# Kernel tuning notes

Measured on AMD Instinct MI355X. Metric: run time of the kernel, lower is better.

Reference implementation:

```python
import jax, jax.numpy as jnp
import numpy as np

N_HEAD = 4
D_MODEL = 256
FEAT_DIM = 256
D_K = D_MODEL // N_HEAD  # 64
TEMP = float(np.sqrt(D_K))
LN_EPS = 1e-5


def setup_inputs() -> dict:
    key = jax.random.key(0)
    ks = jax.random.split(key, 12)
    B, N_src, N_ngh = 2048, 1, 128
    src = jax.random.normal(ks[0], (B, N_src, FEAT_DIM), dtype=jnp.float32)
    seq = jax.random.normal(ks[1], (B, N_ngh, FEAT_DIM), dtype=jnp.float32)
    mask = jax.random.randint(ks[2], (B, N_ngh), 0, 2) > 0
    s_qk = np.sqrt(2.0 / (D_MODEL + D_K))
    w_qs = jax.random.normal(ks[3], (N_HEAD * D_K, D_MODEL), dtype=jnp.float32) * s_qk
    w_ks = jax.random.normal(ks[4], (N_HEAD * D_K, D_MODEL), dtype=jnp.float32) * s_qk
    w_vs = jax.random.normal(ks[5], (N_HEAD * D_K, D_MODEL), dtype=jnp.float32) * s_qk
    fc_w = jax.random.normal(ks[6], (D_MODEL, N_HEAD * D_K), dtype=jnp.float32) * 0.05
    fc_b = jnp.zeros((D_MODEL,), dtype=jnp.float32)
    ln_g = jnp.ones((D_MODEL,), dtype=jnp.float32)
    ln_b = jnp.zeros((D_MODEL,), dtype=jnp.float32)
    fc1_w = jax.random.normal(ks[7], (FEAT_DIM, 2 * D_MODEL), dtype=jnp.float32) * 0.05
    fc1_b = jnp.zeros((FEAT_DIM,), dtype=jnp.float32)
    fc2_w = jax.random.normal(ks[8], (FEAT_DIM, FEAT_DIM), dtype=jnp.float32) * 0.05
    fc2_b = jnp.zeros((FEAT_DIM,), dtype=jnp.float32)
    return {"src": src, "seq": seq, "mask": mask, "w_qs": w_qs, "w_ks": w_ks,
            "w_vs": w_vs, "fc_w": fc_w, "fc_b": fc_b, "ln_g": ln_g, "ln_b": ln_b,
            "fc1_w": fc1_w, "fc1_b": fc1_b, "fc2_w": fc2_w, "fc2_b": fc2_b}


def _forward(src, seq, mask, w_qs, w_ks, w_vs, fc_w, fc_b, ln_g, ln_b,
             fc1_w, fc1_b, fc2_w, fc2_b):
    B, N_src, _ = src.shape
    N_ngh = seq.shape[1]
    nn_ = N_ngh // N_src
    # projections (dropout is identity in eval mode)
    qh = (src @ w_qs.T).reshape(B, N_src, N_HEAD, D_K)              # bshd
    kh = (seq @ w_ks.T).reshape(B, N_src, nn_, N_HEAD, D_K)        # bsnhd
    vh = (seq @ w_vs.T).reshape(B, N_src, nn_, N_HEAD, D_K)
    scores = jnp.einsum('bshd,bsnhd->bshn', qh, kh) / TEMP          # [B,Ns,H,nn]
    # Replicate original mask layout exactly: attn rows are flat in (b,s,h)
    # order, but mask was built with .repeat(n_head,1,1) -> head-major tiling.
    flat = scores.reshape(B * N_src * N_HEAD, nn_)
    mask_rep = jnp.tile(mask.reshape(B * N_src, nn_), (N_HEAD, 1))  # [H*B*Ns, nn]
    flat = jnp.where(mask_rep, -1e10, flat)
    attn = jax.nn.softmax(flat, axis=-1).reshape(B, N_src, N_HEAD, nn_)
    out = jnp.einsum('bshn,bsnhd->bshd', attn, vh).reshape(B, N_src, N_HEAD * D_K)
    out = out @ fc_w.T + fc_b
    x = out + src  # residual (q == src since pos_dim == 0)
    mu = jnp.mean(x, axis=-1, keepdims=True)
    var = jnp.mean(jnp.square(x - mu), axis=-1, keepdims=True)
    x = (x - mu) * jax.lax.rsqrt(var + LN_EPS) * ln_g + ln_b
    # MergeLayer (non_linear=True)
    h = jax.nn.relu(jnp.concatenate([x, src], axis=-1) @ fc1_w.T + fc1_b)
    z = h @ fc2_w.T + fc2_b                                        # [B,Ns,feat]
    return z, attn


def reference(src, seq, mask, w_qs, w_ks, w_vs, fc_w, fc_b, ln_g, ln_b,
              fc1_w, fc1_b, fc2_w, fc2_b):
    return _forward(src, seq, mask, w_qs, w_ks, w_vs, fc_w, fc_b, ln_g, ln_b,
                    fc1_w, fc1_b, fc2_w, fc2_b)
```

## Files before the change

kernel.cpp:

```cpp
#include <hip/hip_runtime.h>

typedef unsigned int uint32;
typedef unsigned short ushort16;

#define DI __device__ __forceinline__

#define BATCH 2048
#define NN    128
#define DM    256
#define NH    4
#define DK    64

#define GLOAD_LDS16(g, s) \
  __builtin_amdgcn_global_load_lds( \
      (const __attribute__((address_space(1))) unsigned int*)(g), \
      (__attribute__((address_space(3))) unsigned int*)(s), 16, 0, 0)

DI float bf2f(ushort16 h) { return __uint_as_float(((uint32)h) << 16); }

DI ushort16 f2bf(float f) {
    uint32 u = __float_as_uint(f);
    uint32 r = u + 0x7fffu + ((u >> 16) & 1u);
    return (ushort16)(r >> 16);
}

DI void unpack8(const uint4 v, float f[8]) {
    f[0] = __uint_as_float(v.x << 16);
    f[1] = __uint_as_float(v.x & 0xffff0000u);
    f[2] = __uint_as_float(v.y << 16);
    f[3] = __uint_as_float(v.y & 0xffff0000u);
    f[4] = __uint_as_float(v.z << 16);
    f[5] = __uint_as_float(v.z & 0xffff0000u);
    f[6] = __uint_as_float(v.w << 16);
    f[7] = __uint_as_float(v.w & 0xffff0000u);
}

DI float dot8(const float* a, const float f[8], float acc) {
    acc = fmaf(a[0], f[0], acc);
    acc = fmaf(a[1], f[1], acc);
    acc = fmaf(a[2], f[2], acc);
    acc = fmaf(a[3], f[3], acc);
    acc = fmaf(a[4], f[4], acc);
    acc = fmaf(a[5], f[5], acc);
    acc = fmaf(a[6], f[6], acc);
    acc = fmaf(a[7], f[7], acc);
    return acc;
}

#define WOFF_QS  0
#define WOFF_KS  65536
#define WOFF_VS  131072
#define WOFF_FC  196608
#define WOFF_FC1 262144
#define WOFF_FC2 393216

__global__ __launch_bounds__(256) void prep_kernel(
    const float* __restrict__ wqs, const float* __restrict__ wks,
    const float* __restrict__ wvs, const float* __restrict__ fcw,
    const float* __restrict__ fc1w, const float* __restrict__ fc2w,
    ushort16* __restrict__ out)
{
    const int bid = blockIdx.x;
    const int t   = threadIdx.x;
    if (bid >= 64 && bid < 128) {
        int base = (bid - 64) * 1024 + t * 4;
        float4 v = *(const float4*)(wks + base);
        int r = base >> 8, c = base & 255;
        out[WOFF_KS + (size_t)(c + 0) * 256 + r] = f2bf(v.x);
        out[WOFF_KS + (size_t)(c + 1) * 256 + r] = f2bf(v.y);
        out[WOFF_KS + (size_t)(c + 2) * 256 + r] = f2bf(v.z);
        out[WOFF_KS + (size_t)(c + 3) * 256 + r] = f2bf(v.w);
        return;
    }
    const float* srcp; size_t soff, doff;
    if (bid < 64)       { srcp = wqs;  soff = (size_t)bid * 1024;         doff = WOFF_QS;  }
    else if (bid < 192) { srcp = wvs;  soff = (size_t)(bid - 128) * 1024; doff = WOFF_VS;  }
    else if (bid < 256) { srcp = fcw;  soff = (size_t)(bid - 192) * 1024; doff = WOFF_FC;  }
    else if (bid < 384) { srcp = fc1w; soff = (size_t)(bid - 256) * 1024; doff = WOFF_FC1; }
    else                { srcp = fc2w; soff = (size_t)(bid - 384) * 1024; doff = WOFF_FC2; }
    float4 v = *(const float4*)(srcp + soff + t * 4);
    uint2 pk;
    pk.x = (uint32)f2bf(v.x) | ((uint32)f2bf(v.y) << 16);
    pk.y = (uint32)f2bf(v.z) | ((uint32)f2bf(v.w) << 16);
    *(uint2*)(out + doff + soff + t * 4) = pk;
}

__global__ __launch_bounds__(256) void qu_kernel(
    const float* __restrict__ src, const ushort16* __restrict__ wbf,
    float* __restrict__ u)
{
    __shared__ float sS[4][DM];
    __shared__ float sQ[4][DM];
    const int t  = threadIdx.x;
    const int b0 = blockIdx.x * 4;

    #pragma unroll
    for (int r = 0; r < 4; ++r) sS[r][t] = src[(size_t)(b0 + r) * DM + t];
    __syncthreads();

    {
        float acc[4] = {0.f,0.f,0.f,0.f};
        const ushort16* wrow = wbf + WOFF_QS + (size_t)t * DM;
        #pragma unroll 2
        for (int kc = 0; kc < DM; kc += 8) {
            uint4 w8 = *(const uint4*)(wrow + kc);
            float wf[8]; unpack8(w8, wf);
            #pragma unroll
            for (int r = 0; r < 4; ++r) acc[r] = dot8(&sS[r][kc], wf, acc[r]);
        }
        #pragma unroll
        for (int r = 0; r < 4; ++r) sQ[r][t] = acc[r];
    }
    __syncthreads();

    const ushort16* wr2 = wbf + WOFF_KS + (size_t)t * DM;
    #pragma unroll
    for (int h = 0; h < NH; ++h) {
        float ua[4] = {0.f,0.f,0.f,0.f};
        #pragma unroll 2
        for (int dc = 0; dc < DK; dc += 8) {
            uint4 w8 = *(const uint4*)(wr2 + h * DK + dc);
            float wf[8]; unpack8(w8, wf);
            #pragma unroll
            for (int r = 0; r < 4; ++r) ua[r] = dot8(&sQ[r][h * DK + dc], wf, ua[r]);
        }
        #pragma unroll
        for (int r = 0; r < 4; ++r)
            u[(size_t)(b0 + r) * (NH * DM) + h * DM + t] = ua[r] * 0.125f;
    }
}

#define USTRIDE 276

__global__ __launch_bounds__(512) void attn_kernel(
    const float* __restrict__ seq, const int* __restrict__ mask,
    const float* __restrict__ u, float* __restrict__ c,
    float* __restrict__ attn_out)
{
    __shared__ float sq[NN * DM];
    __shared__ float sU[NH * USTRIDE];
    __shared__ float sM[8][4];
    __shared__ float sSg[8][4];

    const int t = threadIdx.x;
    const int b = blockIdx.x;
    const int w = t >> 6, l = t & 63;
    const int ln = l >> 2, h = l & 3;

    if (t < 256) {
        float4 v = *(const float4*)(u + (size_t)b * 1024 + t * 4);
        int hh = t >> 6, j = (t & 63) * 4;
        *(float4*)&sU[hh * USTRIDE + j] = v;
    }
    __syncthreads();

    const float* sp = seq + (size_t)b * (NN * DM);
    #pragma unroll
    for (int i = 0; i < 16; ++i) {
        const int r = w * 16 + i;
        const float* ga = sp + r * DM + ((l ^ (r & 7)) << 2);
        GLOAD_LDS16(ga, &sq[r * DM]);
    }
    asm volatile("s_waitcnt vmcnt(0)" ::: "memory");
    __builtin_amdgcn_sched_barrier(0);

    const int rr = w * 16 + ln;
    float s = 0.f;
    {
        const float* urow = &sU[h * USTRIDE];
        const int rsw = rr & 7;
        #pragma unroll 8
        for (int g = 0; g < 64; ++g) {
            float4 sv = *(const float4*)&sq[rr * DM + ((g ^ rsw) << 2)];
            float4 uv = *(const float4*)&urow[g * 4];
            s = fmaf(uv.x, sv.x, s);
            s = fmaf(uv.y, sv.y, s);
            s = fmaf(uv.z, sv.z, s);
            s = fmaf(uv.w, sv.w, s);
        }
    }
    {
        int mr = (4 * b + h) & (BATCH - 1);
        if (mask[(size_t)mr * NN + rr] != 0) s = -1e10f;
    }
    float m = s;
    m = fmaxf(m, __shfl_xor(m, 4));
    m = fmaxf(m, __shfl_xor(m, 8));
    m = fmaxf(m, __shfl_xor(m, 16));
    m = fmaxf(m, __shfl_xor(m, 32));
    float ev = __expf(s - m);
    float sg = ev;
    sg += __shfl_xor(sg, 4);
    sg += __shfl_xor(sg, 8);
    sg += __shfl_xor(sg, 16);
    sg += __shfl_xor(sg, 32);

    float cc[4][4];
    #pragma unroll
    for (int hh = 0; hh < 4; ++hh) {
        cc[hh][0] = 0.f; cc[hh][1] = 0.f; cc[hh][2] = 0.f; cc[hh][3] = 0.f;
    }
    #pragma unroll
    for (int i = 0; i < 16; ++i) {
        float e0 = __shfl(ev, i * 4 + 0);
        float e1 = __shfl(ev, i * 4 + 1);
        float e2 = __shfl(ev, i * 4 + 2);
        float e3 = __shfl(ev, i * 4 + 3);
        const int r = w * 16 + i;
        float4 sv = *(const float4*)&sq[r * DM + ((l ^ (r & 7)) << 2)];
        cc[0][0] = fmaf(e0, sv.x, cc[0][0]); cc[0][1] = fmaf(e0, sv.y, cc[0][1]);
        cc[0][2] = fmaf(e0, sv.z, cc[0][2]); cc[0][3] = fmaf(e0, sv.w, cc[0][3]);
        cc[1][0] = fmaf(e1, sv.x, cc[1][0]); cc[1][1] = fmaf(e1, sv.y, cc[1][1]);
        cc[1][2] = fmaf(e1, sv.z, cc[1][2]); cc[1][3] = fmaf(e1, sv.w, cc[1][3]);
        cc[2][0] = fmaf(e2, sv.x, cc[2][0]); cc[2][1] = fmaf(e2, sv.y, cc[2][1]);
        cc[2][2] = fmaf(e2, sv.z, cc[2][2]); cc[2][3] = fmaf(e2, sv.w, cc[2][3]);
        cc[3][0] = fmaf(e3, sv.x, cc[3][0]); cc[3][1] = fmaf(e3, sv.y, cc[3][1]);
        cc[3][2] = fmaf(e3, sv.z, cc[3][2]); cc[3][3] = fmaf(e3, sv.w, cc[3][3]);
    }

    #pragma unroll
    for (int hh = 0; hh < 4; ++hh) {
        #pragma unroll
        for (int k = 0; k < 4; ++k)
            sq[w * 4096 + hh * 256 + l * 4 + k] = cc[hh][k];
    }
    if (l < 4) { sM[w][l] = m; sSg[w][l] = sg; }
    __syncthreads();

    {
        float M = sM[0][h];
        #pragma unroll
        for (int w2 = 1; w2 < 8; ++w2) M = fmaxf(M, sM[w2][h]);
        float S = 0.f;
        #pragma unroll
        for (int w2 = 0; w2 < 8; ++w2) S += sSg[w2][h] * __expf(sM[w2][h] - M);
        float p = ev * __expf(m - M) / S;
        attn_out[(size_t)b * (NH * NN) + h * NN + rr] = p;
    }

    #pragma unroll
    for (int rep = 0; rep < 2; ++rep) {
        int idx = t + rep * 512;
        int hh = idx >> 8, j = idx & 255;
        float M = sM[0][hh];
        #pragma unroll
        for (int w2 = 1; w2 < 8; ++w2) M = fmaxf(M, sM[w2][hh]);
        float S = 0.f, acc = 0.f;
        #pragma unroll
        for (int w2 = 0; w2 < 8; ++w2) {
            float sc = __expf(sM[w2][hh] - M);
            S   += sSg[w2][hh] * sc;
            acc += sq[w2 * 4096 + hh * 256 + j] * sc;
        }
        c[(size_t)b * 1024 + idx] = acc / S;
    }
}

__global__ __launch_bounds__(256) void mlp_kernel(
    const float* __restrict__ c, const float* __restrict__ src,
    const ushort16* __restrict__ wbf,
    const float* __restrict__ fcb, const float* __restrict__ lng,
    const float* __restrict__ lnb, const float* __restrict__ fc1b,
    const float* __restrict__ fc2b, float* __restrict__ zout)
{
    __shared__ float sC[8][1024];
    __shared__ float sA[8][256];
    __shared__ float sX[8][256];
    __shared__ float sS[8][256];
    __shared__ float sH[8][256];
    __shared__ float sRed[4][8][2];

    const int t  = threadIdx.x;
    const int b0 = blockIdx.x * 8;
    const int h  = t >> 6;

    #pragma unroll
    for (int i = 0; i < 8; ++i)
        *(float4*)&sC[i][t * 4] = *(const float4*)&c[(size_t)(b0 + i) * 1024 + t * 4];
    #pragma unroll
    for (int r = 0; r < 8; ++r) sS[r][t] = src[(size_t)(b0 + r) * DM + t];
    __syncthreads();

    {
        float acc[8] = {0.f,0.f,0.f,0.f,0.f,0.f,0.f,0.f};
        const ushort16* wr = wbf + WOFF_VS + (size_t)t * DM;
        for (int kc = 0; kc < DM; kc += 8) {
            uint4 w8 = *(const uint4*)(wr + kc);
            float wf[8]; unpack8(w8, wf);
            #pragma unroll
            for (int r = 0; r < 8; ++r) acc[r] = dot8(&sC[r][h * 256 + kc], wf, acc[r]);
        }
        #pragma unroll
        for (int r = 0; r < 8; ++r) sA[r][t] = acc[r];
    }
    __syncthreads();

    float xv[8];
    {
        float acc[8] = {0.f,0.f,0.f,0.f,0.f,0.f,0.f,0.f};
        const ushort16* wr = wbf + WOFF_FC + (size_t)t * DM;
        for (int kc = 0; kc < DM; kc += 8) {
            uint4 w8 = *(const uint4*)(wr + kc);
            float wf[8]; unpack8(w8, wf);
            #pragma unroll
            for (int r = 0; r < 8; ++r) acc[r] = dot8(&sA[r][kc], wf, acc[r]);
        }
        float bb = fcb[t];
        #pragma unroll
        for (int r = 0; r < 8; ++r) xv[r] = acc[r] + bb + sS[r][t];
    }
    {
        const int w = t >> 6, l = t & 63;
        #pragma unroll
        for (int r = 0; r < 8; ++r) {
            float vs = xv[r], vq = xv[r] * xv[r];
            #pragma unroll
            for (int o = 32; o > 0; o >>= 1) {
                vs += __shfl_xor(vs, o, 64);
                vq += __shfl_xor(vq, o, 64);
            }
            if (l == 0) { sRed[w][r][0] = vs; sRed[w][r][1] = vq; }
        }
        __syncthreads();
        float g = lng[t], bb = lnb[t];
        #pragma unroll
        for (int r = 0; r < 8; ++r) {
            float S = sRed[0][r][0] + sRed[1][r][0] + sRed[2][r][0] + sRed[3][r][0];
            float Q = sRed[0][r][1] + sRed[1][r][1] + sRed[2][r][1] + sRed[3][r][1];
            float mu  = S * (1.f / 256.f);
            float var = Q * (1.f / 256.f) - mu * mu;
            float rs  = rsqrtf(var + 1e-5f);
            sX[r][t] = (xv[r] - mu) * rs * g + bb;
        }
    }
    __syncthreads();

    {
        float acc[8] = {0.f,0.f,0.f,0.f,0.f,0.f,0.f,0.f};
        const ushort16* wr = wbf + WOFF_FC1 + (size_t)t * 512;
        for (int kc = 0; kc < 256; kc += 8) {
            uint4 w8 = *(const uint4*)(wr + kc);
            float wf[8]; unpack8(w8, wf);
            #pragma unroll
            for (int r = 0; r < 8; ++r) acc[r] = dot8(&sX[r][kc], wf, acc[r]);
        }
        for (int kc = 0; kc < 256; kc += 8) {
            uint4 w8 = *(const uint4*)(wr + 256 + kc);
            float wf[8]; unpack8(w8, wf);
            #pragma unroll
            for (int r = 0; r < 8; ++r) acc[r] = dot8(&sS[r][kc], wf, acc[r]);
        }
        float bb = fc1b[t];
        #pragma unroll
        for (int r = 0; r < 8; ++r) sH[r][t] = fmaxf(acc[r] + bb, 0.f);
    }
    __syncthreads();

    {
        float acc[8] = {0.f,0.f,0.f,0.f,0.f,0.f,0.f,0.f};
        const ushort16* wr = wbf + WOFF_FC2 + (size_t)t * DM;
        for (int kc = 0; kc < DM; kc += 8) {
            uint4 w8 = *(const uint4*)(wr + kc);
            float wf[8]; unpack8(w8, wf);
            #pragma unroll
            for (int r = 0; r < 8; ++r) acc[r] = dot8(&sH[r][kc], wf, acc[r]);
        }
        float bb = fc2b[t];
        #pragma unroll
        for (int r = 0; r < 8; ++r)
            zout[(size_t)(b0 + r) * DM + t] = acc[r] + bb;
    }
}

extern "C" void kernel_launch(void* const* d_in, const int* in_sizes, int n_in,
                              void* d_out, int out_size, void* d_ws, size_t ws_size,
                              hipStream_t stream)
{
    const float* src  = (const float*)d_in[0];
    const float* seq  = (const float*)d_in[1];
    const int*   mask = (const int*)d_in[2];
    const float* wqs  = (const float*)d_in[3];
    const float* wks  = (const float*)d_in[4];
    const float* wvs  = (const float*)d_in[5];
    const float* fcw  = (const float*)d_in[6];
    const float* fcb  = (const float*)d_in[7];
    const float* lng  = (const float*)d_in[8];
    const float* lnb  = (const float*)d_in[9];
    const float* fc1w = (const float*)d_in[10];
    const float* fc1b = (const float*)d_in[11];
    const float* fc2w = (const float*)d_in[12];
    const float* fc2b = (const float*)d_in[13];

    float* zout     = (float*)d_out;
    float* attn_out = zout + (size_t)BATCH * DM;

    float* u = (float*)d_ws;
    float* cbuf = u + (size_t)BATCH * 1024;
    ushort16* wbf = (ushort16*)(cbuf + (size_t)BATCH * 1024);

    prep_kernel<<<448, 256, 0, stream>>>(wqs, wks, wvs, fcw, fc1w, fc2w, wbf);
    qu_kernel<<<512, 256, 0, stream>>>(src, wbf, u);
    attn_kernel<<<BATCH, 512, 0, stream>>>(seq, mask, u, cbuf, attn_out);
    mlp_kernel<<<256, 256, 0, stream>>>(cbuf, src, wbf, fcb, lng, lnb,
                                        fc1b, fc2b, zout);
}
```

Before: 465.6 us.

## Fuse query projection into attention kernel with double-buffered streaming online softmax

Removes the separate qu_kernel and computes q and u = Wk^T q per batch row inside the attention kernel, so the u workspace round trip and one launch go away. The neighbour rows are now streamed in four chunks through a two-buffer LDS ring with partial vmcnt waits, and an online softmax with per-head running max and sum is kept across chunks. This cuts LDS use from 128 KB to about 64 KB per block, so more blocks can be resident, and overlaps loads with compute. The cost is that each block recomputes the small projection GEMVs from bf16 weights, and there is more readlane and rescaling work per chunk.

```diff
diff --git a/kernel.cpp b/kernel.cpp
--- a/kernel.cpp
+++ b/kernel.cpp
@@ -16,7 +16,16 @@
       (const __attribute__((address_space(1))) unsigned int*)(g), \
       (__attribute__((address_space(3))) unsigned int*)(s), 16, 0, 0)
 
-DI float bf2f(ushort16 h) { return __uint_as_float(((uint32)h) << 16); }
+#define WAIT_VMCNT(n) do { \
+    asm volatile("s_waitcnt vmcnt(" #n ")" ::: "memory"); \
+    __builtin_amdgcn_sched_barrier(0); \
+  } while (0)
+
+#define CFENCE() asm volatile("" ::: "memory")
+
+DI float readl(float v, int lane) {
+    return __uint_as_float(__builtin_amdgcn_readlane(__float_as_uint(v), lane));
+}
 
 DI ushort16 f2bf(float f) {
     uint32 u = __float_as_uint(f);
@@ -85,157 +94,187 @@
     *(uint2*)(out + doff + soff + t * 4) = pk;
 }
 
-__global__ __launch_bounds__(256) void qu_kernel(
-    const float* __restrict__ src, const ushort16* __restrict__ wbf,
-    float* __restrict__ u)
+#define USTRIDE 276
+
+__global__ __launch_bounds__(512, 4) void attn_fused_kernel(
+    const float* __restrict__ src, const float* __restrict__ seq,
+    const int* __restrict__ mask, const ushort16* __restrict__ wbf,
+    float* __restrict__ c, float* __restrict__ attn_out)
 {
-    __shared__ float sS[4][DM];
-    __shared__ float sQ[4][DM];
-    const int t  = threadIdx.x;
-    const int b0 = blockIdx.x * 4;
-
-    #pragma unroll
-    for (int r = 0; r < 4; ++r) sS[r][t] = src[(size_t)(b0 + r) * DM + t];
-    __syncthreads();
-
-    {
-        float acc[4] = {0.f,0.f,0.f,0.f};
-        const ushort16* wrow = wbf + WOFF_QS + (size_t)t * DM;
-        #pragma unroll 2
-        for (int kc = 0; kc < DM; kc += 8) {
-            uint4 w8 = *(const uint4*)(wrow + kc);
-            float wf[8]; unpack8(w8, wf);
-            #pragma unroll
-            for (int r = 0; r < 4; ++r) acc[r] = dot8(&sS[r][kc], wf, acc[r]);
-        }
-        #pragma unroll
-        for (int r = 0; r < 4; ++r) sQ[r][t] = acc[r];
-    }
-    __syncthreads();
-
-    const ushort16* wr2 = wbf + WOFF_KS + (size_t)t * DM;
-    #pragma unroll
-    for (int h = 0; h < NH; ++h) {
-        float ua[4] = {0.f,0.f,0.f,0.f};
-        #pragma unroll 2
-        for (int dc = 0; dc < DK; dc += 8) {
-            uint4 w8 = *(const uint4*)(wr2 + h * DK + dc);
-            float wf[8]; unpack8(w8, wf);
-            #pragma unroll
-            for (int r = 0; r < 4; ++r) ua[r] = dot8(&sQ[r][h * DK + dc], wf, ua[r]);
-        }
-        #pragma unroll
-        for (int r = 0; r < 4; ++r)
-            u[(size_t)(b0 + r) * (NH * DM) + h * DM + t] = ua[r] * 0.125f;
-    }
-}
-
-#define USTRIDE 276
-
-__global__ __launch_bounds__(512) void attn_kernel(
-    const float* __restrict__ seq, const int* __restrict__ mask,
-    const float* __restrict__ u, float* __restrict__ c,
-    float* __restrict__ attn_out)
-{
-    __shared__ float sq[NN * DM];
-    __shared__ float sU[NH * USTRIDE];
-    __shared__ float sM[8][4];
-    __shared__ float sSg[8][4];
+    __shared__ __align__(16) float sq_[16384];
+    __shared__ __align__(16) float sU[NH * USTRIDE];
+    __shared__ __align__(16) float sQ[256];
+    __shared__ int   sMk[512];
+    __shared__ __align__(16) float sM[8][4];
+    __shared__ __align__(16) float sSg[8][4];
 
     const int t = threadIdx.x;
     const int b = blockIdx.x;
     const int w = t >> 6, l = t & 63;
-    const int ln = l >> 2, h = l & 3;
+    const int rq = l >> 4;
+    const int myh = (l >> 2) & 3;
+    const int kseg = l & 3;
+
+    const float* sp = seq + (size_t)b * (NN * DM);
+    float* wsl = &sq_[w * 2048];
+
+    {
+        int hh = t >> 7, n = t & 127;
+        int mr = (4 * b + hh) & (BATCH - 1);
+        sMk[t] = mask[(size_t)mr * NN + n];
+    }
 
     if (t < 256) {
-        float4 v = *(const float4*)(u + (size_t)b * 1024 + t * 4);
-        int hh = t >> 6, j = (t & 63) * 4;
-        *(float4*)&sU[hh * USTRIDE + j] = v;
-    }
-    __syncthreads();
-
-    const float* sp = seq + (size_t)b * (NN * DM);
-    #pragma unroll
-    for (int i = 0; i < 16; ++i) {
-        const int r = w * 16 + i;
-        const float* ga = sp + r * DM + ((l ^ (r & 7)) << 2);
-        GLOAD_LDS16(ga, &sq[r * DM]);
-    }
-    asm volatile("s_waitcnt vmcnt(0)" ::: "memory");
-    __builtin_amdgcn_sched_barrier(0);
-
-    const int rr = w * 16 + ln;
-    float s = 0.f;
-    {
-        const float* urow = &sU[h * USTRIDE];
-        const int rsw = rr & 7;
-        #pragma unroll 8
-        for (int g = 0; g < 64; ++g) {
-            float4 sv = *(const float4*)&sq[rr * DM + ((g ^ rsw) << 2)];
-            float4 uv = *(const float4*)&urow[g * 4];
-            s = fmaf(uv.x, sv.x, s);
-            s = fmaf(uv.y, sv.y, s);
-            s = fmaf(uv.z, sv.z, s);
-            s = fmaf(uv.w, sv.w, s);
-        }
-    }
-    {
-        int mr = (4 * b + h) & (BATCH - 1);
-        if (mask[(size_t)mr * NN + rr] != 0) s = -1e10f;
-    }
-    float m = s;
-    m = fmaxf(m, __shfl_xor(m, 4));
-    m = fmaxf(m, __shfl_xor(m, 8));
-    m = fmaxf(m, __shfl_xor(m, 16));
-    m = fmaxf(m, __shfl_xor(m, 32));
-    float ev = __expf(s - m);
-    float sg = ev;
-    sg += __shfl_xor(sg, 4);
-    sg += __shfl_xor(sg, 8);
-    sg += __shfl_xor(sg, 16);
-    sg += __shfl_xor(sg, 32);
-
-    float cc[4][4];
-    #pragma unroll
-    for (int hh = 0; hh < 4; ++hh) {
-        cc[hh][0] = 0.f; cc[hh][1] = 0.f; cc[hh][2] = 0.f; cc[hh][3] = 0.f;
-    }
-    #pragma unroll
-    for (int i = 0; i < 16; ++i) {
-        float e0 = __shfl(ev, i * 4 + 0);
-        float e1 = __shfl(ev, i * 4 + 1);
-        float e2 = __shfl(ev, i * 4 + 2);
-        float e3 = __shfl(ev, i * 4 + 3);
-        const int r = w * 16 + i;
-        float4 sv = *(const float4*)&sq[r * DM + ((l ^ (r & 7)) << 2)];
-        cc[0][0] = fmaf(e0, sv.x, cc[0][0]); cc[0][1] = fmaf(e0, sv.y, cc[0][1]);
-        cc[0][2] = fmaf(e0, sv.z, cc[0][2]); cc[0][3] = fmaf(e0, sv.w, cc[0][3]);
-        cc[1][0] = fmaf(e1, sv.x, cc[1][0]); cc[1][1] = fmaf(e1, sv.y, cc[1][1]);
-        cc[1][2] = fmaf(e1, sv.z, cc[1][2]); cc[1][3] = fmaf(e1, sv.w, cc[1][3]);
-        cc[2][0] = fmaf(e2, sv.x, cc[2][0]); cc[2][1] = fmaf(e2, sv.y, cc[2][1]);
-        cc[2][2] = fmaf(e2, sv.z, cc[2][2]); cc[2][3] = fmaf(e2, sv.w, cc[2][3]);
-        cc[3][0] = fmaf(e3, sv.x, cc[3][0]); cc[3][1] = fmaf(e3, sv.y, cc[3][1]);
-        cc[3][2] = fmaf(e3, sv.z, cc[3][2]); cc[3][3] = fmaf(e3, sv.w, cc[3][3]);
-    }
-
-    #pragma unroll
-    for (int hh = 0; hh < 4; ++hh) {
-        #pragma unroll
-        for (int k = 0; k < 4; ++k)
-            sq[w * 4096 + hh * 256 + l * 4 + k] = cc[hh][k];
-    }
-    if (l < 4) { sM[w][l] = m; sSg[w][l] = sg; }
-    __syncthreads();
-
-    {
-        float M = sM[0][h];
-        #pragma unroll
-        for (int w2 = 1; w2 < 8; ++w2) M = fmaxf(M, sM[w2][h]);
-        float S = 0.f;
-        #pragma unroll
-        for (int w2 = 0; w2 < 8; ++w2) S += sSg[w2][h] * __expf(sM[w2][h] - M);
-        float p = ev * __expf(m - M) / S;
-        attn_out[(size_t)b * (NH * NN) + h * NN + rr] = p;
+        float acc = 0.f;
+        const ushort16* wrow = wbf + WOFF_QS + (size_t)t * DM;
+        const float* srow = src + (size_t)b * DM;
+        #pragma unroll 4
+        for (int kc = 0; kc < DM; kc += 8) {
+            uint4 w8 = *(const uint4*)(wrow + kc);
+            float wf[8]; unpack8(w8, wf);
+            float4 sa = *(const float4*)(srow + kc);
+            float4 sb = *(const float4*)(srow + kc + 4);
+            acc = fmaf(sa.x, wf[0], acc); acc = fmaf(sa.y, wf[1], acc);
+            acc = fmaf(sa.z, wf[2], acc); acc = fmaf(sa.w, wf[3], acc);
+            acc = fmaf(sb.x, wf[4], acc); acc = fmaf(sb.y, wf[5], acc);
+            acc = fmaf(sb.z, wf[6], acc); acc = fmaf(sb.w, wf[7], acc);
+        }
+        sQ[t] = acc;
+    }
+    __syncthreads();
+
+    {
+        const int cc2 = t & 255;
+        const int h1  = t >> 8;
+        float a0 = 0.f, a1 = 0.f;
+        const ushort16* wr2 = wbf + WOFF_KS + (size_t)cc2 * DM;
+        #pragma unroll 2
+        for (int dc = 0; dc < DK; dc += 8) {
+            uint4 wA = *(const uint4*)(wr2 + h1 * DK + dc);
+            uint4 wB = *(const uint4*)(wr2 + (h1 + 2) * DK + dc);
+            float fA[8], fB[8]; unpack8(wA, fA); unpack8(wB, fB);
+            a0 = dot8(&sQ[h1 * DK + dc], fA, a0);
+            a1 = dot8(&sQ[(h1 + 2) * DK + dc], fB, a1);
+        }
+        sU[h1 * USTRIDE + cc2]       = a0 * 0.125f;
+        sU[(h1 + 2) * USTRIDE + cc2] = a1 * 0.125f;
+    }
+    __syncthreads();
+
+    float m0 = -1e30f, m1 = -1e30f, m2 = -1e30f, m3 = -1e30f;
+    float sr0 = 0.f, sr1 = 0.f, sr2 = 0.f, sr3 = 0.f;
+    float4 cc0 = {0,0,0,0}, cc1 = {0,0,0,0}, cc2v = {0,0,0,0}, cc3 = {0,0,0,0};
+    float shist0 = 0.f, shist1 = 0.f, shist2 = 0.f, shist3 = 0.f;
+
+    auto issue = [&](int kk, int bufoff) {
+        CFENCE();
+        #pragma unroll
+        for (int i = 0; i < 4; ++i) {
+            const int r = (w << 4) + kk * 4 + i;
+            const int cp = l ^ (((r & 3) << 1) ^ rq);
+            GLOAD_LDS16(sp + r * 256 + cp * 4, wsl + bufoff + i * 256);
+        }
+    };
+
+    auto process = [&](int kk, int bufoff, float& sh) {
+        const int r_my = (w << 4) + kk * 4 + rq;
+        float s = 0.f;
+        {
+            const float* rowb = wsl + bufoff + rq * 256;
+            const float* urow = &sU[myh * USTRIDE];
+            const int sk = ((r_my & 3) << 1) ^ kseg;
+            #pragma unroll
+            for (int jj = 0; jj < 16; ++jj) {
+                const int cidx = (kseg << 4) | jj;
+                const int cp = cidx ^ sk;
+                float4 sv = *(const float4*)(rowb + cp * 4);
+                float4 uv = *(const float4*)(urow + cidx * 4);
+                s = fmaf(uv.x, sv.x, s); s = fmaf(uv.y, sv.y, s);
+                s = fmaf(uv.z, sv.z, s); s = fmaf(uv.w, sv.w, s);
+            }
+        }
+        s += __shfl_xor(s, 1, 64);
+        s += __shfl_xor(s, 2, 64);
+        if (sMk[myh * 128 + r_my] != 0) s = -1e10f;
+        sh = s;
+        float bmax = s;
+        bmax = fmaxf(bmax, __shfl_xor(bmax, 16, 64));
+        bmax = fmaxf(bmax, __shfl_xor(bmax, 32, 64));
+        float bh0 = readl(bmax, 0), bh1 = readl(bmax, 4);
+        float bh2 = readl(bmax, 8), bh3 = readl(bmax, 12);
+        float n0 = fmaxf(m0, bh0), n1 = fmaxf(m1, bh1);
+        float n2 = fmaxf(m2, bh2), n3 = fmaxf(m3, bh3);
+        float f0 = __expf(m0 - n0), f1 = __expf(m1 - n1);
+        float f2 = __expf(m2 - n2), f3 = __expf(m3 - n3);
+        sr0 *= f0; sr1 *= f1; sr2 *= f2; sr3 *= f3;
+        cc0.x *= f0; cc0.y *= f0; cc0.z *= f0; cc0.w *= f0;
+        cc1.x *= f1; cc1.y *= f1; cc1.z *= f1; cc1.w *= f1;
+        cc2v.x *= f2; cc2v.y *= f2; cc2v.z *= f2; cc2v.w *= f2;
+        cc3.x *= f3; cc3.y *= f3; cc3.z *= f3; cc3.w *= f3;
+        m0 = n0; m1 = n1; m2 = n2; m3 = n3;
+        float nm = (myh == 0) ? n0 : (myh == 1) ? n1 : (myh == 2) ? n2 : n3;
+        float e = __expf(s - nm);
+        #pragma unroll
+        for (int i = 0; i < 4; ++i) {
+            const int r2 = (w << 4) + kk * 4 + i;
+            const int cp = l ^ (((r2 & 3) << 1) ^ rq);
+            float4 sv = *(const float4*)(wsl + bufoff + i * 256 + cp * 4);
+            float e0 = readl(e, (i << 4) | 0);
+            float e1 = readl(e, (i << 4) | 4);
+            float e2 = readl(e, (i << 4) | 8);
+            float e3 = readl(e, (i << 4) | 12);
+            sr0 += e0; sr1 += e1; sr2 += e2; sr3 += e3;
+            cc0.x = fmaf(e0, sv.x, cc0.x); cc0.y = fmaf(e0, sv.y, cc0.y);
+            cc0.z = fmaf(e0, sv.z, cc0.z); cc0.w = fmaf(e0, sv.w, cc0.w);
+            cc1.x = fmaf(e1, sv.x, cc1.x); cc1.y = fmaf(e1, sv.y, cc1.y);
+            cc1.z = fmaf(e1, sv.z, cc1.z); cc1.w = fmaf(e1, sv.w, cc1.w);
+            cc2v.x = fmaf(e2, sv.x, cc2v.x); cc2v.y = fmaf(e2, sv.y, cc2v.y);
+            cc2v.z = fmaf(e2, sv.z, cc2v.z); cc2v.w = fmaf(e2, sv.w, cc2v.w);
+            cc3.x = fmaf(e3, sv.x, cc3.x); cc3.y = fmaf(e3, sv.y, cc3.y);
+            cc3.z = fmaf(e3, sv.z, cc3.z); cc3.w = fmaf(e3, sv.w, cc3.w);
+        }
+        CFENCE();
+    };
+
+    issue(0, 0);
+    issue(1, 1024);
+    WAIT_VMCNT(4);
+    process(0, 0, shist0);
+    issue(2, 0);
+    WAIT_VMCNT(4);
+    process(1, 1024, shist1);
+    issue(3, 1024);
+    WAIT_VMCNT(4);
+    process(2, 0, shist2);
+    WAIT_VMCNT(0);
+    process(3, 1024, shist3);
+
+    CFENCE();
+    *(float4*)(wsl + 0 * 256 + l * 4) = cc0;
+    *(float4*)(wsl + 1 * 256 + l * 4) = cc1;
+    *(float4*)(wsl + 2 * 256 + l * 4) = cc2v;
+    *(float4*)(wsl + 3 * 256 + l * 4) = cc3;
+    if (l == 0) {
+        *(float4*)&sM[w][0]  = make_float4(m0, m1, m2, m3);
+        *(float4*)&sSg[w][0] = make_float4(sr0, sr1, sr2, sr3);
+    }
+    __syncthreads();
+
+    {
+        float Mh = sM[0][myh];
+        #pragma unroll
+        for (int w2 = 1; w2 < 8; ++w2) Mh = fmaxf(Mh, sM[w2][myh]);
+        float Sh = 0.f;
+        #pragma unroll
+        for (int w2 = 0; w2 < 8; ++w2) Sh += sSg[w2][myh] * __expf(sM[w2][myh] - Mh);
+        if (kseg == 0) {
+            float inv = 1.f / Sh;
+            size_t base = (size_t)b * (NH * NN) + myh * NN + (w << 4) + rq;
+            attn_out[base + 0]  = __expf(shist0 - Mh) * inv;
+            attn_out[base + 4]  = __expf(shist1 - Mh) * inv;
+            attn_out[base + 8]  = __expf(shist2 - Mh) * inv;
+            attn_out[base + 12] = __expf(shist3 - Mh) * inv;
+        }
     }
 
     #pragma unroll
@@ -250,7 +289,7 @@
         for (int w2 = 0; w2 < 8; ++w2) {
             float sc = __expf(sM[w2][hh] - M);
             S   += sSg[w2][hh] * sc;
-            acc += sq[w2 * 4096 + hh * 256 + j] * sc;
+            acc += sq_[w2 * 2048 + hh * 256 + j] * sc;
         }
         c[(size_t)b * 1024 + idx] = acc / S;
     }
@@ -394,13 +433,12 @@
     float* zout     = (float*)d_out;
     float* attn_out = zout + (size_t)BATCH * DM;
 
-    float* u = (float*)d_ws;
-    float* cbuf = u + (size_t)BATCH * 1024;
+    float* cbuf = (float*)d_ws;
     ushort16* wbf = (ushort16*)(cbuf + (size_t)BATCH * 1024);
 
     prep_kernel<<<448, 256, 0, stream>>>(wqs, wks, wvs, fcw, fc1w, fc2w, wbf);
-    qu_kernel<<<512, 256, 0, stream>>>(src, wbf, u);
-    attn_kernel<<<BATCH, 512, 0, stream>>>(seq, mask, u, cbuf, attn_out);
+    attn_fused_kernel<<<BATCH, 512, 0, stream>>>(src, seq, mask, wbf,
+                                                 cbuf, attn_out);
     mlp_kernel<<<256, 256, 0, stream>>>(cbuf, src, wbf, fcb, lng, lnb,
                                         fc1b, fc2b, zout);
 }
```

Result: slower. 477.3 us (+2.5%).
